# Optimization experiments

Measured on AMD Instinct MI355X. Metric: run time of the kernel, lower is better.

The kernel has to match this reference:

```python
import jax, jax.numpy as jnp
import numpy as np

B, N, DIM = 4, 8192, 512
HEADS, DHEAD = 8, 64
INNER = HEADS * DHEAD          # 512
M = 256                        # num landmarks
L = N // M                     # tokens per landmark group (n % m == 0 -> no pad)
ITERS = 6                      # Moore-Penrose iterations
KRES = 33                      # residual depthwise conv kernel (along n)
SCALE = DHEAD ** -0.5


def setup_inputs() -> dict:
    key = jax.random.key(0)
    k1, k2, k3, k4 = jax.random.split(key, 4)
    return {
        "x": jax.random.normal(k1, (B, N, DIM), jnp.float32),
        "w_qkv": jax.random.normal(k2, (DIM, 3 * INNER), jnp.float32) * (DIM ** -0.5),
        "w_out": jax.random.normal(k3, (INNER, DIM), jnp.float32) * (INNER ** -0.5),
        "b_out": jnp.zeros((DIM,), jnp.float32),
        "res_kernel": jax.random.normal(k4, (HEADS, 1, KRES, 1), jnp.float32) * 0.05,
    }


def _moore_penrose_pinv(x, iters=ITERS):
    # x: (b, h, m, m)
    abs_x = jnp.abs(x)
    col = abs_x.sum(axis=-1)
    row = abs_x.sum(axis=-2)
    z = jnp.swapaxes(x, -1, -2) / (jnp.max(col) * jnp.max(row))
    I = jnp.eye(x.shape[-1], dtype=x.dtype)
    for _ in range(iters):
        xz = x @ z
        z = 0.25 * z @ (13 * I - xz @ (15 * I - xz @ (7 * I - xz)))
    return z


def reference(x, w_qkv, w_out, b_out, res_kernel):
    b, n, _ = x.shape
    qkv = x @ w_qkv                               # (b, n, 3*inner)
    q, k, v = jnp.split(qkv, 3, axis=-1)
    to_heads = lambda t: t.reshape(b, n, HEADS, DHEAD).transpose(0, 2, 1, 3)  # (b,h,n,d)
    q, k, v = to_heads(q), to_heads(k), to_heads(v)
    q = q * SCALE

    # landmarks: mean over consecutive groups of L tokens -> (b,h,M,d)
    q_l = q.reshape(b, HEADS, M, L, DHEAD).sum(axis=3) / L
    k_l = k.reshape(b, HEADS, M, L, DHEAD).sum(axis=3) / L

    attn1 = jax.nn.softmax(jnp.einsum('bhid,bhjd->bhij', q, k_l), axis=-1)    # (b,h,n,M)
    attn2 = jax.nn.softmax(jnp.einsum('bhid,bhjd->bhij', q_l, k_l), axis=-1)  # (b,h,M,M)
    attn3 = jax.nn.softmax(jnp.einsum('bhid,bhjd->bhij', q_l, k), axis=-1)    # (b,h,M,n)

    out = attn1 @ _moore_penrose_pinv(attn2) @ (attn3 @ v)                    # (b,h,n,d)

    # depthwise residual conv over the sequence axis, per head
    res = jax.lax.conv_general_dilated(
        v, res_kernel, window_strides=(1, 1),
        padding=[(KRES // 2, KRES // 2), (0, 0)],
        dimension_numbers=('NCHW', 'OIHW', 'NCHW'),
        feature_group_count=HEADS)
    out = out + res

    out = out.transpose(0, 2, 1, 3).reshape(b, n, INNER)
    return out @ w_out + b_out
```

## Files before the change

### kernel.cpp

```cpp
#include <hip/hip_runtime.h>
#include <stdint.h>
#include <stddef.h>


typedef __bf16 bf16x8 __attribute__((ext_vector_type(8)));
typedef __bf16 bf16x4 __attribute__((ext_vector_type(4)));
typedef float f32x4 __attribute__((ext_vector_type(4)));

__device__ __forceinline__ f32x4 mfma_bf16(bf16x8 a, bf16x8 b, f32x4 c) {
    return __builtin_amdgcn_mfma_f32_16x16x32_bf16(a, b, c, 0, 0, 0);
}

__device__ __forceinline__ void gload16(const __bf16* g, __bf16* l) {
    __builtin_amdgcn_global_load_lds(
        (const __attribute__((address_space(1))) void*)g,
        (__attribute__((address_space(3))) void*)l, 16, 0, 0);
}

__global__ __launch_bounds__(256) void k_cvt(const float* __restrict__ in,
        __bf16* __restrict__ out, float* __restrict__ stats) {
    if (blockIdx.x == 0 && threadIdx.x == 0) { stats[0] = 1.f; stats[1] = 0.f; }
    size_t base = ((size_t)blockIdx.x * 256 + threadIdx.x) * 8;
    float4 a = *(const float4*)&in[base];
    float4 b = *(const float4*)&in[base + 4];
    bf16x8 o;
    o[0] = (__bf16)a.x; o[1] = (__bf16)a.y; o[2] = (__bf16)a.z; o[3] = (__bf16)a.w;
    o[4] = (__bf16)b.x; o[5] = (__bf16)b.y; o[6] = (__bf16)b.z; o[7] = (__bf16)b.w;
    *(bf16x8*)&out[base] = o;
}

__global__ __launch_bounds__(256) void k_transpose_f32(const float* __restrict__ in,
        __bf16* __restrict__ out, int R, int C) {
    __shared__ __bf16 tile[64 * 72];
    int r0 = blockIdx.x * 64, c0 = blockIdx.y * 64;
    int tid = threadIdx.x;
    #pragma unroll
    for (int i = 0; i < 16; ++i) {
        int slot = i * 256 + tid;
        int rr = slot >> 6, cc = slot & 63;
        tile[rr * 72 + cc] = (__bf16)in[(size_t)(r0 + rr) * C + c0 + cc];
    }
    __syncthreads();
    #pragma unroll
    for (int i = 0; i < 2; ++i) {
        int slot = i * 256 + tid;
        int cc = slot >> 3, s = slot & 7;
        bf16x8 t;
        #pragma unroll
        for (int j = 0; j < 8; ++j) t[j] = tile[(s * 8 + j) * 72 + cc];
        *(bf16x8*)&out[(size_t)(c0 + cc) * R + r0 + s * 8] = t;
    }
}

__global__ __launch_bounds__(256) void k_transpose_bf(const __bf16* __restrict__ in,
        __bf16* __restrict__ out, int R, int C, long bsi, long bso) {
    __shared__ __bf16 tile[64 * 72];
    in  += (size_t)blockIdx.z * bsi;
    out += (size_t)blockIdx.z * bso;
    int r0 = blockIdx.x * 64, c0 = blockIdx.y * 64;
    int tid = threadIdx.x;
    #pragma unroll
    for (int i = 0; i < 2; ++i) {
        int slot = i * 256 + tid;
        int rr = slot >> 3, s = slot & 7;
        *(bf16x8*)&tile[rr * 72 + s * 8] =
            *(const bf16x8*)&in[(size_t)(r0 + rr) * C + c0 + s * 8];
    }
    __syncthreads();
    #pragma unroll
    for (int i = 0; i < 2; ++i) {
        int slot = i * 256 + tid;
        int cc = slot >> 3, s = slot & 7;
        bf16x8 t;
        #pragma unroll
        for (int j = 0; j < 8; ++j) t[j] = tile[(s * 8 + j) * 72 + cc];
        *(bf16x8*)&out[(size_t)(c0 + cc) * R + r0 + s * 8] = t;
    }
}

template<int MODE>
__global__ __launch_bounds__(256) void k_gemm_big(const __bf16* __restrict__ A,
        const __bf16* __restrict__ Bt, int K,
        __bf16* __restrict__ qp, __bf16* __restrict__ kp, __bf16* __restrict__ vp,
        float* __restrict__ outp, const float* __restrict__ bias) {
    __shared__ __bf16 sA[128 * 64];
    __shared__ __bf16 sB[128 * 64];
    constexpr int NT  = (MODE == 0) ? 12 : 4;
    constexpr int TOT = (MODE == 0) ? 3072 : 1024;
    int flat = blockIdx.x;
    int t = (flat & 7) * (TOT / 8) + (flat >> 3);
    int m0 = (t / NT) * 128, n0 = (t % NT) * 128;
    int tid = threadIdx.x;
    int wave = tid >> 6, l = tid & 63, lm = l & 15, lq = l >> 4;
    int wm = wave & 1, wn = wave >> 1;
    int lr = l >> 3, lc8 = l & 7;
    int src_c = (lc8 ^ lr) * 8;
    f32x4 acc[4][4] = {};
    for (int k0 = 0; k0 < K; k0 += 64) {
        #pragma unroll
        for (int i = 0; i < 4; ++i) {
            int g = wave * 4 + i;
            gload16(&A[(size_t)(m0 + g * 8 + lr) * K + k0 + src_c], &sA[g * 512]);
        }
        #pragma unroll
        for (int i = 0; i < 4; ++i) {
            int g = wave * 4 + i;
            gload16(&Bt[(size_t)(n0 + g * 8 + lr) * K + k0 + src_c], &sB[g * 512]);
        }
        __syncthreads();
// ... 12 lines not shown
                bfr[ni] = *(bf16x8*)&sB[r * 64 + ((ch ^ (r & 7)) << 3)];
            }
            #pragma unroll
            for (int mi = 0; mi < 4; ++mi)
                #pragma unroll
                for (int ni = 0; ni < 4; ++ni)
                    acc[mi][ni] = mfma_bf16(af[mi], bfr[ni], acc[mi][ni]);
        }
        __syncthreads();
    }
    #pragma unroll
    for (int mi = 0; mi < 4; ++mi)
    #pragma unroll
    for (int ni = 0; ni < 4; ++ni)
    #pragma unroll
    for (int reg = 0; reg < 4; ++reg) {
        int gr = m0 + wm * 64 + mi * 16 + lq * 4 + reg;
        int gc = n0 + wn * 64 + ni * 16 + lm;
        float v = acc[mi][ni][reg];
        if (MODE == 0) {
            int which = gc >> 9, rem = gc & 511;
            int h = rem >> 6, d = rem & 63;
            int b = gr >> 13, tok = gr & 8191;
            size_t dst = ((size_t)((b * 8 + h) * 8192 + tok)) * 64 + d;
            if (which == 0)      qp[dst] = (__bf16)(v * 0.125f);
            else if (which == 1) kp[dst] = (__bf16)v;
            else                 vp[dst] = (__bf16)v;
        } else {
            outp[(size_t)gr * 512 + gc] = v + bias[gc];
        }
    }
}

__global__ __launch_bounds__(256) void k_landmarks(const __bf16* __restrict__ q,
        const __bf16* __restrict__ k, __bf16* __restrict__ ql, __bf16* __restrict__ kl) {
    int idx = blockIdx.x * 256 + threadIdx.x;
    int sel = idx >> 19;
    int rem = idx & 524287;
    int bh = rem >> 14;
    int m  = (rem >> 6) & 255;
    int d  = rem & 63;
    const __bf16* src = sel ? k : q;
    __bf16* dst = sel ? kl : ql;
    const __bf16* p = src + ((size_t)(bh * 8192 + m * 32)) * 64 + d;
    float s = 0.f;
    #pragma unroll
    for (int j = 0; j < 32; ++j) s += (float)p[j * 64];
    dst[(size_t)bh * 16384 + m * 64 + d] = (__bf16)(s * (1.f / 32.f));
}

__global__ __launch_bounds__(256) void k_attn2(const __bf16* __restrict__ ql,
        const __bf16* __restrict__ kl, __bf16* __restrict__ ph, __bf16* __restrict__ pl) {
    int tid = threadIdx.x;
    int wave = tid >> 6, l = tid & 63, lm = l & 15, lq = l >> 4;
    int bh = blockIdx.y;
    int r0 = blockIdx.x * 64 + wave * 16;
    const __bf16* qb = ql + (size_t)bh * 16384;
    const __bf16* kb = kl + (size_t)bh * 16384;
    bf16x8 af[2];
    #pragma unroll
    for (int ko = 0; ko < 2; ++ko)
        af[ko] = *(const bf16x8*)&qb[(size_t)(r0 + lm) * 64 + ko * 32 + lq * 8];
    f32x4 S[16] = {};
    #pragma unroll
    for (int ci = 0; ci < 16; ++ci)
        #pragma unroll
        for (int ko = 0; ko < 2; ++ko) {
            bf16x8 bfr = *(const bf16x8*)&kb[(size_t)(ci * 16 + lm) * 64 + ko * 32 + lq * 8];
            S[ci] = mfma_bf16(af[ko], bfr, S[ci]);
        }
    __bf16* oh = ph + (size_t)bh * 65536;
    __bf16* ol = pl + (size_t)bh * 65536;
    #pragma unroll
    for (int reg = 0; reg < 4; ++reg) {
        float sum = 0.f;
        #pragma unroll
        for (int ci = 0; ci < 16; ++ci) {
            float e = __expf(S[ci][reg]); S[ci][reg] = e; sum += e;
        }
        #pragma unroll
        for (int msk = 1; msk < 16; msk <<= 1) sum += __shfl_xor(sum, msk);
        float inv = 1.f / sum;
        int row = r0 + lq * 4 + reg;
        #pragma unroll
        for (int ci = 0; ci < 16; ++ci) {
            float v = S[ci][reg] * inv;
            __bf16 hh = (__bf16)v;
            oh[(size_t)row * 256 + ci * 16 + lm] = hh;
            ol[(size_t)row * 256 + ci * 16 + lm] = (__bf16)(v - (float)hh);
        }
    }
}

__global__ __launch_bounds__(256) void k_stats(const __bf16* __restrict__ ph,
        const __bf16* __restrict__ pl, float* stats) {
    __shared__ float red[256];
    int tid = threadIdx.x;
    const __bf16* a = ph + (size_t)blockIdx.x * 65536;
    const __bf16* b = pl + (size_t)blockIdx.x * 65536;
    float cs = 0.f;
    for (int r = 0; r < 256; ++r)
        cs += (float)a[r * 256 + tid] + (float)b[r * 256 + tid];
    red[tid] = cs; __syncthreads();
    for (int off = 128; off > 0; off >>= 1) {
        if (tid < off) red[tid] = fmaxf(red[tid], red[tid + off]);
        __syncthreads();
    }
    if (tid == 0) atomicMax((int*)&stats[1], __float_as_int(red[0]));
}

__global__ __launch_bounds__(256) void k_z0(const __bf16* __restrict__ ph,
        const __bf16* __restrict__ pl, const float* __restrict__ stats,
        __bf16* __restrict__ zh, __bf16* __restrict__ zl) {
    int idx = blockIdx.x * 256 + threadIdx.x;
    int bh = idx >> 16, r = (idx >> 8) & 255, c = idx & 255;
    float inv = 1.f / (stats[0] * stats[1]);
    size_t src = ((size_t)bh << 16) + (size_t)c * 256 + r;
    float v = ((float)ph[src] + (float)pl[src]) * inv;
    __bf16 hh = (__bf16)v;
    zh[idx] = hh;
    zl[idx] = (__bf16)(v - (float)hh);
}

__device__ __forceinline__ void pgemm_core(const __bf16* __restrict__ Ah,
        const __bf16* __restrict__ Al, const __bf16* __restrict__ Bth,
        const __bf16* __restrict__ Btl, int m0, int n0,
        __bf16* sAh, __bf16* sAl, __bf16* sBh, __bf16* sBl, f32x4 acc[2]) {
    int tid = threadIdx.x;
    int wave = tid >> 6, l = tid & 63, lm = l & 15, lq = l >> 4;
    int wm = wave & 1, wn = wave >> 1;
    int lr = l >> 3, lc8 = l & 7;
    int src_c = (lc8 ^ lr) * 8;
    for (int k0 = 0; k0 < 256; k0 += 64) {
        {
            size_t ra = (size_t)(m0 + wave * 8 + lr) * 256 + k0 + src_c;
            gload16(&Ah[ra], &sAh[wave * 512]);
            gload16(&Al[ra], &sAl[wave * 512]);
        }
        #pragma unroll
        for (int i = 0; i < 2; ++i) {
            int g = wave * 2 + i;
            size_t rb = (size_t)(n0 + g * 8 + lr) * 256 + k0 + src_c;
            gload16(&Bth[rb], &sBh[g * 512]);
            gload16(&Btl[rb], &sBl[g * 512]);
        }
        __syncthreads();
        #pragma unroll
        for (int ko = 0; ko < 2; ++ko) {
            int ch = (ko << 2) | lq;
            int rA = wm * 16 + lm;
            int oA = rA * 64 + ((ch ^ (rA & 7)) << 3);
            bf16x8 a_h = *(bf16x8*)&sAh[oA];
            bf16x8 a_l = *(bf16x8*)&sAl[oA];
            bf16x8 b_h[2], b_l[2];
            #pragma unroll
            for (int ni = 0; ni < 2; ++ni) {
                int r = wn * 32 + ni * 16 + lm;
                int o = r * 64 + ((ch ^ (r & 7)) << 3);
                b_h[ni] = *(bf16x8*)&sBh[o];
                b_l[ni] = *(bf16x8*)&sBl[o];
            }
            #pragma unroll
            for (int ni = 0; ni < 2; ++ni) {
                acc[ni] = mfma_bf16(a_h, b_h[ni], acc[ni]);
                acc[ni] = mfma_bf16(a_h, b_l[ni], acc[ni]);
                acc[ni] = mfma_bf16(a_l, b_h[ni], acc[ni]);
            }
        }
        __syncthreads();
    }
}

__global__ __launch_bounds__(256) void k_pgemm(const __bf16* __restrict__ Ah,
        const __bf16* __restrict__ Al, const __bf16* __restrict__ Bth,
        const __bf16* __restrict__ Btl, const __bf16* __restrict__ Ch,
        const __bf16* __restrict__ Cl, __bf16* __restrict__ OutH,
        __bf16* __restrict__ OutL, float alpha, const float* __restrict__ sPtr,
        float beta, float delta, int outMode, long bStride) {
    __shared__ __bf16 sAh[32 * 64], sAl[32 * 64], sBh[64 * 64], sBl[64 * 64];
    int tid = threadIdx.x;
    int wave = tid >> 6, l = tid & 63, lm = l & 15, lq = l >> 4;
    int wm = wave & 1, wn = wave >> 1;
    int total = gridDim.x;
    int flat = blockIdx.x;
    int t = (flat & 7) * (total >> 3) + (flat >> 3);
    int ntb = total >> 8;
    int tpb = ntb << 3;
    int bh = t / tpb, rem = t - bh * tpb;
    int m0 = (rem / ntb) * 32, n0 = (rem % ntb) * 64;
    float aEff = alpha;
    if (sPtr) aEff *= 1.f / (sPtr[0] * sPtr[1]);
    f32x4 acc[2] = {};
    pgemm_core(Ah + (size_t)bh * 65536, Al + (size_t)bh * 65536,
               Bth + (size_t)bh * bStride, Btl + (size_t)bh * bStride,
               m0, n0, sAh, sAl, sBh, sBl, acc);
    #pragma unroll
    for (int ni = 0; ni < 2; ++ni)
    #pragma unroll
    for (int reg = 0; reg < 4; ++reg) {
        int gr = m0 + wm * 16 + lq * 4 + reg;
        int gc = n0 + wn * 32 + ni * 16 + lm;
        float v = aEff * acc[ni][reg];
        if (beta != 0.f) {
            size_t ci = (size_t)bh * 65536 + (size_t)gr * 256 + gc;
            v += beta * ((float)Ch[ci] + (float)Cl[ci]);
        }
        if (gr == gc) v += delta;
        if (outMode == 0) {
            size_t di = (size_t)bh * 65536 + (size_t)gr * 256 + gc;
            __bf16 hh = (__bf16)v;
            OutH[di] = hh;
            OutL[di] = (__bf16)(v - (float)hh);
        } else {
            int ci2 = gr >> 4, lqm = (gr >> 2) & 3, r = gr & 3;
            int slot = ((ci2 >> 1) << 5) + (lqm << 3) + ((ci2 & 1) << 2) + r;
            OutH[(size_t)bh * 16384 + (size_t)gc * 256 + slot] = (__bf16)v;
        }
    }
}

__global__ __launch_bounds__(256) void k_pgemm_dual(const __bf16* __restrict__ Zh,
        const __bf16* __restrict__ Zl, const __bf16* __restrict__ A2h,
        const __bf16* __restrict__ A2l, const __bf16* __restrict__ Bth,
        const __bf16* __restrict__ Btl, __bf16* __restrict__ OzH,
        __bf16* __restrict__ OzL, __bf16* __restrict__ OaH, __bf16* __restrict__ OaL) {
    __shared__ __bf16 sAh[32 * 64], sAl[32 * 64], sBh[64 * 64], sBl[64 * 64];
    int tid = threadIdx.x;
    int wave = tid >> 6, l = tid & 63, lm = l & 15, lq = l >> 4;
    int wm = wave & 1, wn = wave >> 1;
    int total = gridDim.x;
    int flat = blockIdx.x;
    int t = (flat & 7) * (total >> 3) + (flat >> 3);
    int zz = t >> 5, rem = t & 31;
    int m0 = (rem >> 2) * 32, n0 = (rem & 3) * 64;
    int bh = zz & 31;
    const __bf16* Lh = (zz >= 32 ? A2h : Zh) + (size_t)bh * 65536;
    const __bf16* Ll = (zz >= 32 ? A2l : Zl) + (size_t)bh * 65536;
    __bf16* Oh = (zz >= 32 ? OaH : OzH) + (size_t)bh * 65536;
    __bf16* Ol = (zz >= 32 ? OaL : OzL) + (size_t)bh * 65536;
    f32x4 acc[2] = {};
    pgemm_core(Lh, Ll, Bth + (size_t)bh * 65536, Btl + (size_t)bh * 65536,
               m0, n0, sAh, sAl, sBh, sBl, acc);
    #pragma unroll
    for (int ni = 0; ni < 2; ++ni)
    #pragma unroll
    for (int reg = 0; reg < 4; ++reg) {
        int gr = m0 + wm * 16 + lq * 4 + reg;
        int gc = n0 + wn * 32 + ni * 16 + lm;
        float v = 0.25f * acc[ni][reg];
        __bf16 hh = (__bf16)v;
        Oh[(size_t)gr * 256 + gc] = hh;
        Ol[(size_t)gr * 256 + gc] = (__bf16)(v - (float)hh);
    }
}

__global__ __launch_bounds__(256) void k_attn3(const __bf16* __restrict__ ql,
        const __bf16* __restrict__ kk, const __bf16* __restrict__ vt,
        float* __restrict__ O_s, float* __restrict__ l_s) {
    int tid = threadIdx.x;
    int wave = tid >> 6, l = tid & 63, lm = l & 15, lq = l >> 4;
    int s = blockIdx.x, bh = blockIdx.y;
    const __bf16* qb = ql + (size_t)bh * 16384;
    bf16x8 qa[4][2];
    #pragma unroll
    for (int mi = 0; mi < 4; ++mi)
        #pragma unroll
        for (int ko = 0; ko < 2; ++ko)
            qa[mi][ko] = *(const bf16x8*)&qb[(size_t)(wave * 64 + mi * 16 + lm) * 64 + ko * 32 + lq * 8];
    f32x4 O[4][4] = {};
    float lsum[4] = {};
    for (int it = 0; it < 8; ++it) {
        int c0 = s * 512 + it * 64;
        bf16x8 kf[4][2];
        #pragma unroll
        for (int ci = 0; ci < 4; ++ci)
            #pragma unroll
            for (int ko = 0; ko < 2; ++ko)
                kf[ci][ko] = *(const bf16x8*)&kk[((size_t)bh * 8192 + c0 + ci * 16 + lm) * 64 + ko * 32 + lq * 8];
        f32x4 St[4][4] = {};
        #pragma unroll
        for (int ci = 0; ci < 4; ++ci)
            #pragma unroll
            for (int ko = 0; ko < 2; ++ko)
                #pragma unroll
                for (int mi = 0; mi < 4; ++mi)
                    St[mi][ci] = mfma_bf16(kf[ci][ko], qa[mi][ko], St[mi][ci]);
        bf16x4 pk[4][4];
        #pragma unroll
        for (int mi = 0; mi < 4; ++mi)
            #pragma unroll
            for (int ci = 0; ci < 4; ++ci)
                #pragma unroll
                for (int reg = 0; reg < 4; ++reg) {
                    float e = __expf(St[mi][ci][reg]);
                    lsum[mi] += e;
                    pk[mi][ci][reg] = (__bf16)e;
                }
        #pragma unroll
        for (int ko = 0; ko < 2; ++ko) {
            bf16x8 af[4];
            #pragma unroll
            for (int mi = 0; mi < 4; ++mi)
                #pragma unroll
                for (int r = 0; r < 4; ++r) {
                    af[mi][r]     = pk[mi][2 * ko][r];
                    af[mi][4 + r] = pk[mi][2 * ko + 1][r];
                }
            #pragma unroll
            for (int ni = 0; ni < 4; ++ni) {
                const __bf16* vrow = &vt[((size_t)bh * 64 + ni * 16 + lm) * 8192 + c0 + ko * 32 + lq * 4];
                bf16x4 v0 = *(const bf16x4*)&vrow[0];
                bf16x4 v1 = *(const bf16x4*)&vrow[16];
                bf16x8 vb;
                #pragma unroll
                for (int r = 0; r < 4; ++r) { vb[r] = v0[r]; vb[4 + r] = v1[r]; }
                #pragma unroll
                for (int mi = 0; mi < 4; ++mi)
                    O[mi][ni] = mfma_bf16(af[mi], vb, O[mi][ni]);
            }
        }
    }
    #pragma unroll
    for (int mi = 0; mi < 4; ++mi) {
        float v = lsum[mi];
        v += __shfl_xor(v, 16);
        v += __shfl_xor(v, 32);
        lsum[mi] = v;
    }
    int base = (bh * 16 + s) * 256;
    #pragma unroll
    for (int mi = 0; mi < 4; ++mi)
        if (lq == 0) l_s[base + wave * 64 + mi * 16 + lm] = lsum[mi];
    #pragma unroll
    for (int mi = 0; mi < 4; ++mi)
        #pragma unroll
        for (int reg = 0; reg < 4; ++reg) {
            int r = wave * 64 + mi * 16 + lq * 4 + reg;
            #pragma unroll
            for (int ni = 0; ni < 4; ++ni)
                O_s[((size_t)(base + r)) * 64 + ni * 16 + lm] = O[mi][ni][reg];
        }
}

__global__ __launch_bounds__(256) void k_t2combine(const float* __restrict__ O_s,
        const float* __restrict__ l_s, __bf16* __restrict__ t2th,
        __bf16* __restrict__ t2tl) {
    int idx = blockIdx.x * 256 + threadIdx.x;
    int bh = idx >> 14, r = (idx >> 6) & 255, d = idx & 63;
    float den = 0.f, num = 0.f;
    #pragma unroll
    for (int s = 0; s < 16; ++s) {
        int b2 = (bh * 16 + s) * 256 + r;
        den += l_s[b2];
        num += O_s[(size_t)b2 * 64 + d];
    }
    float v = num / den;
    __bf16 hh = (__bf16)v;
    size_t di = ((size_t)bh * 64 + d) * 256 + r;
    t2th[di] = hh;
    t2tl[di] = (__bf16)(v - (float)hh);
}

__global__ __launch_bounds__(256) void k_conv(const __bf16* __restrict__ vt,
        const float* __restrict__ resk, __bf16* __restrict__ convb) {
    int bh = blockIdx.y, h = bh & 7;
    int d = threadIdx.x & 63, tg = threadIdx.x >> 6;
    int t0 = blockIdx.x * 64 + tg * 16;
    __shared__ float kfs[33];
    if (threadIdx.x < 33) kfs[threadIdx.x] = resk[h * 33 + threadIdx.x];
    __syncthreads();
    const __bf16* row = vt + ((size_t)bh * 64 + d) * 8192;
    float win[48];
    #pragma unroll
    for (int c = 0; c < 6; ++c) {
        int tok0 = t0 - 16 + c * 8;
        if (tok0 >= 0 && tok0 + 7 < 8192) {
            bf16x8 v8 = *(const bf16x8*)&row[tok0];
            #pragma unroll
            for (int e = 0; e < 8; ++e) win[c * 8 + e] = (float)v8[e];
        } else {
            #pragma unroll
            for (int e = 0; e < 8; ++e) {
                int tok = tok0 + e;
                win[c * 8 + e] = (tok >= 0 && tok < 8192) ? (float)row[tok] : 0.f;
            }
        }
    }
    float o[16];
    #pragma unroll
    for (int i = 0; i < 16; ++i) o[i] = 0.f;
    #pragma unroll
    for (int j = 0; j < 33; ++j) {
        float kf = kfs[j];
        #pragma unroll
        for (int i = 0; i < 16; ++i) o[i] += kf * win[i + j];
    }
    __bf16* outr = convb + ((size_t)bh * 8192) * 64 + d;
    #pragma unroll
    for (int i = 0; i < 16; ++i)
        outr[(size_t)(t0 + i) * 64] = (__bf16)o[i];
}

__global__ __launch_bounds__(256) void k_attn1(const __bf16* __restrict__ q,
        const __bf16* __restrict__ kl, const __bf16* __restrict__ zt2p,
        const __bf16* __restrict__ convb, __bf16* __restrict__ outp) {
    int tid = threadIdx.x;
    int wave = tid >> 6, l = tid & 63, lm = l & 15, lq = l >> 4;
    int bh = blockIdx.y;
    int t0 = blockIdx.x * 256;
    int b = bh >> 3, h = bh & 7;
    const __bf16* qb = q + (size_t)bh * 8192 * 64;
    const __bf16* kb = kl + (size_t)bh * 16384;
    const __bf16* zb = zt2p + (size_t)bh * 16384;
    int rowb = t0 + wave * 64;
    bf16x8 qa[4][2];
    #pragma unroll
    for (int mi = 0; mi < 4; ++mi)
        #pragma unroll
        for (int ko = 0; ko < 2; ++ko)
            qa[mi][ko] = *(const bf16x8*)&qb[(size_t)(rowb + mi * 16 + lm) * 64 + ko * 32 + lq * 8];
    f32x4 O[4][4] = {};
    float rs[4] = {};
    #pragma unroll
    for (int c2 = 0; c2 < 8; ++c2) {
        bf16x8 kf[2][2];
        #pragma unroll
        for (int ci = 0; ci < 2; ++ci)
            #pragma unroll
            for (int ko = 0; ko < 2; ++ko)
                kf[ci][ko] = *(const bf16x8*)&kb[(size_t)((c2 * 2 + ci) * 16 + lm) * 64 + ko * 32 + lq * 8];
        f32x4 St[4][2] = {};
        #pragma unroll
        for (int ci = 0; ci < 2; ++ci)
// ... 67 lines not shown
        off += (bytes + 255) & ~(size_t)255;
        return p;
    };
    const size_t PL = 2097152;
    __bf16* q_bf   = (__bf16*)alloc(33554432);
    __bf16* k_bf   = (__bf16*)alloc(33554432);
    __bf16* vt     = (__bf16*)alloc(33554432);
    __bf16* outpre = (__bf16*)alloc(33554432);
    __bf16* q_l    = (__bf16*)alloc(1048576);
    __bf16* k_l    = (__bf16*)alloc(1048576);
    __bf16* a2h    = (__bf16*)alloc(8388608);
    __bf16* zAh    = (__bf16*)alloc(8388608);
    __bf16* zBh    = (__bf16*)alloc(8388608);
    __bf16* Amh    = (__bf16*)alloc(8388608);
    __bf16* W2h    = (__bf16*)alloc(8388608);
    __bf16* W3h    = (__bf16*)alloc(8388608);
    float*  O_s    = (float*)alloc(33554432);
    float*  l_s    = (float*)alloc(524288);
    __bf16* t2th   = (__bf16*)alloc(2097152);
    __bf16* zt2t   = (__bf16*)alloc(1048576);
    __bf16* wqkvt  = (__bf16*)alloc(1572864);
    __bf16* woutt  = (__bf16*)alloc(524288);
    float*  stats  = (float*)alloc(256);
    __bf16* convb  = (__bf16*)O_s;
    __bf16* xb     = (__bf16*)O_s;
    __bf16* a2l = a2h + PL;
    __bf16* zAl = zAh + PL;
    __bf16* zBl = zBh + PL;
    __bf16* Aml = Amh + PL;
    __bf16* W2l = W2h + PL;
    __bf16* W3l = W3h + PL;
    __bf16* t2tl = t2th + 524288;

    k_cvt<<<8192, 256, 0, stream>>>(x, xb, stats);
    k_transpose_f32<<<dim3(8, 24), 256, 0, stream>>>(wqkv, wqkvt, 512, 1536);
    k_transpose_f32<<<dim3(8, 8), 256, 0, stream>>>(wout, woutt, 512, 512);
    k_gemm_big<0><<<3072, 256, 0, stream>>>(xb, wqkvt, 512,
            q_bf, k_bf, outpre, nullptr, nullptr);
    k_transpose_bf<<<dim3(128, 1, 32), 256, 0, stream>>>(outpre, vt, 8192, 64, 524288, 524288);
    k_landmarks<<<4096, 256, 0, stream>>>(q_bf, k_bf, q_l, k_l);
    k_attn2<<<dim3(4, 32), 256, 0, stream>>>(q_l, k_l, a2h, a2l);
    k_stats<<<32, 256, 0, stream>>>(a2h, a2l, stats);
    k_z0<<<8192, 256, 0, stream>>>(a2h, a2l, stats, zAh, zAl);
    k_attn3<<<dim3(16, 32), 256, 0, stream>>>(q_l, k_bf, vt, O_s, l_s);
    k_t2combine<<<2048, 256, 0, stream>>>(O_s, l_s, t2th, t2tl);
    k_conv<<<dim3(128, 32), 256, 0, stream>>>(vt, resk, convb);
    k_pgemm<<<1024, 256, 0, stream>>>(a2h, a2l, a2h, a2l,
            nullptr, nullptr, Amh, Aml, 1.f, stats, 0.f, 0.f, 0, 65536);
    __bf16 *zch = zAh, *zcl = zAl, *znh = zBh, *znl = zBl;
    __bf16 *Ach = Amh, *Acl = Aml, *Anh = a2h, *Anl = a2l;
    for (int it = 0; it < 6; ++it) {
        k_pgemm<<<1024, 256, 0, stream>>>(Ach, Acl, Ach, Acl,
                Ach, Acl, W2h, W2l, 1.f, nullptr, -7.f, 15.f, 0, 65536);
        k_pgemm<<<1024, 256, 0, stream>>>(Ach, Acl, W2h, W2l,
                nullptr, nullptr, W3h, W3l, -1.f, nullptr, 0.f, 13.f, 0, 65536);
        if (it < 5) {
            k_pgemm_dual<<<2048, 256, 0, stream>>>(zch, zcl, Ach, Acl,
                    W3h, W3l, znh, znl, Anh, Anl);
            __bf16* t;
            t = Ach; Ach = Anh; Anh = t;
            t = Acl; Acl = Anl; Anl = t;
        } else {
            k_pgemm_dual<<<1024, 256, 0, stream>>>(zch, zcl, zch, zcl,
                    W3h, W3l, znh, znl, znh, znl);
        }
        __bf16* t;
        t = zch; zch = znh; znh = t;
        t = zcl; zcl = znl; znl = t;
    }
    k_pgemm<<<256, 256, 0, stream>>>(zch, zcl, t2th, t2tl,
            nullptr, nullptr, zt2t, nullptr, 1.f, nullptr, 0.f, 0.f, 1, 16384);
    k_attn1<<<dim3(32, 32), 256, 0, stream>>>(q_bf, k_l, zt2t, convb, outpre);
    k_gemm_big<1><<<1024, 256, 0, stream>>>(outpre, woutt, 512,
            nullptr, nullptr, nullptr, (float*)d_out, bout);
}
```

Baseline: 642.0 us.

## Merge independent small kernels into combined launches sharing a block-index dispatch

Several independent stages are folded into multi-role kernels that pick their work by block index: input conversion with both weight transposes, the V transpose with landmark pooling, and the attn3/z0/first pgemm, t2combine/W2, and W3/conv pairs. The first iteration's W2 and W3 products are hoisted out of the Newton loop into these combined launches. The aim is to cut launch count and tail idle time by letting unrelated work fill the GPU together. In exchange, heterogeneous blocks share one launch configuration, so register and LDS use is set by the heaviest role and may lower occupancy for the lighter ones.

```diff
diff --git a/kernel.cpp b/kernel.cpp
--- a/kernel.cpp
+++ b/kernel.cpp
@@ -17,10 +17,10 @@
         (__attribute__((address_space(3))) void*)l, 16, 0, 0);
 }
 
-__global__ __launch_bounds__(256) void k_cvt(const float* __restrict__ in,
-        __bf16* __restrict__ out, float* __restrict__ stats) {
-    if (blockIdx.x == 0 && threadIdx.x == 0) { stats[0] = 1.f; stats[1] = 0.f; }
-    size_t base = ((size_t)blockIdx.x * 256 + threadIdx.x) * 8;
+
+__device__ __forceinline__ void cvt_body(int bid, const float* __restrict__ in,
+        __bf16* __restrict__ out) {
+    size_t base = ((size_t)bid * 256 + threadIdx.x) * 8;
     float4 a = *(const float4*)&in[base];
     float4 b = *(const float4*)&in[base + 4];
     bf16x8 o;
@@ -29,10 +29,9 @@
     *(bf16x8*)&out[base] = o;
 }
 
-__global__ __launch_bounds__(256) void k_transpose_f32(const float* __restrict__ in,
-        __bf16* __restrict__ out, int R, int C) {
-    __shared__ __bf16 tile[64 * 72];
-    int r0 = blockIdx.x * 64, c0 = blockIdx.y * 64;
+__device__ __forceinline__ void tf32_body(const float* __restrict__ in,
+        __bf16* __restrict__ out, int R, int C, int bx, int by, __bf16* tile) {
+    int r0 = bx * 64, c0 = by * 64;
     int tid = threadIdx.x;
     #pragma unroll
     for (int i = 0; i < 16; ++i) {
@@ -52,19 +51,18 @@
     }
 }
 
-__global__ __launch_bounds__(256) void k_transpose_bf(const __bf16* __restrict__ in,
-        __bf16* __restrict__ out, int R, int C, long bsi, long bso) {
-    __shared__ __bf16 tile[64 * 72];
-    in  += (size_t)blockIdx.z * bsi;
-    out += (size_t)blockIdx.z * bso;
-    int r0 = blockIdx.x * 64, c0 = blockIdx.y * 64;
+__device__ __forceinline__ void tbf_body(const __bf16* __restrict__ in0,
+        __bf16* __restrict__ out0, int bx, int bz, __bf16* tile) {
+    const __bf16* in = in0 + (size_t)bz * 524288;
+    __bf16* out = out0 + (size_t)bz * 524288;
+    int r0 = bx * 64, c0 = 0;
     int tid = threadIdx.x;
     #pragma unroll
     for (int i = 0; i < 2; ++i) {
         int slot = i * 256 + tid;
         int rr = slot >> 3, s = slot & 7;
         *(bf16x8*)&tile[rr * 72 + s * 8] =
-            *(const bf16x8*)&in[(size_t)(r0 + rr) * C + c0 + s * 8];
+            *(const bf16x8*)&in[(size_t)(r0 + rr) * 64 + c0 + s * 8];
     }
     __syncthreads();
     #pragma unroll
@@ -74,7 +72,293 @@
         bf16x8 t;
         #pragma unroll
         for (int j = 0; j < 8; ++j) t[j] = tile[(s * 8 + j) * 72 + cc];
-        *(bf16x8*)&out[(size_t)(c0 + cc) * R + r0 + s * 8] = t;
+        *(bf16x8*)&out[(size_t)(c0 + cc) * 8192 + r0 + s * 8] = t;
+    }
+}
+
+__device__ __forceinline__ void landmarks_body(int idx, const __bf16* __restrict__ q,
+        const __bf16* __restrict__ k, __bf16* __restrict__ ql, __bf16* __restrict__ kl) {
+    int sel = idx >> 19;
+    int rem = idx & 524287;
+    int bh = rem >> 14;
+    int m  = (rem >> 6) & 255;
+    int d  = rem & 63;
+    const __bf16* src = sel ? k : q;
+    __bf16* dst = sel ? kl : ql;
+    const __bf16* p = src + ((size_t)(bh * 8192 + m * 32)) * 64 + d;
+    float s = 0.f;
+    #pragma unroll
+    for (int j = 0; j < 32; ++j) s += (float)p[j * 64];
+    dst[(size_t)bh * 16384 + m * 64 + d] = (__bf16)(s * (1.f / 32.f));
+}
+
+__device__ __forceinline__ void z0_body(int idx, const __bf16* __restrict__ ph,
+        const __bf16* __restrict__ pl, const float* __restrict__ stats,
+        __bf16* __restrict__ zh, __bf16* __restrict__ zl) {
+    int bh = idx >> 16, r = (idx >> 8) & 255, c = idx & 255;
+    float inv = 1.f / (stats[0] * stats[1]);
+    size_t src = ((size_t)bh << 16) + (size_t)c * 256 + r;
+    float v = ((float)ph[src] + (float)pl[src]) * inv;
+    __bf16 hh = (__bf16)v;
+    zh[idx] = hh;
+    zl[idx] = (__bf16)(v - (float)hh);
+}
+
+__device__ __forceinline__ void pgemm_core(const __bf16* __restrict__ Ah,
+        const __bf16* __restrict__ Al, const __bf16* __restrict__ Bth,
+        const __bf16* __restrict__ Btl, int m0, int n0,
+        __bf16* sAh, __bf16* sAl, __bf16* sBh, __bf16* sBl, f32x4 acc[2]) {
+    int tid = threadIdx.x;
+    int wave = tid >> 6, l = tid & 63, lm = l & 15, lq = l >> 4;
+    int wm = wave & 1, wn = wave >> 1;
+    int lr = l >> 3, lc8 = l & 7;
+    int src_c = (lc8 ^ lr) * 8;
+    for (int k0 = 0; k0 < 256; k0 += 64) {
+        {
+            size_t ra = (size_t)(m0 + wave * 8 + lr) * 256 + k0 + src_c;
+            gload16(&Ah[ra], &sAh[wave * 512]);
+            gload16(&Al[ra], &sAl[wave * 512]);
+        }
+        #pragma unroll
+        for (int i = 0; i < 2; ++i) {
+            int g = wave * 2 + i;
+            size_t rb = (size_t)(n0 + g * 8 + lr) * 256 + k0 + src_c;
+            gload16(&Bth[rb], &sBh[g * 512]);
+            gload16(&Btl[rb], &sBl[g * 512]);
+        }
+        __syncthreads();
+        #pragma unroll
+        for (int ko = 0; ko < 2; ++ko) {
+            int ch = (ko << 2) | lq;
+            int rA = wm * 16 + lm;
+            int oA = rA * 64 + ((ch ^ (rA & 7)) << 3);
+            bf16x8 a_h = *(bf16x8*)&sAh[oA];
+            bf16x8 a_l = *(bf16x8*)&sAl[oA];
+            bf16x8 b_h[2], b_l[2];
+            #pragma unroll
+            for (int ni = 0; ni < 2; ++ni) {
+                int r = wn * 32 + ni * 16 + lm;
+                int o = r * 64 + ((ch ^ (r & 7)) << 3);
+                b_h[ni] = *(bf16x8*)&sBh[o];
+                b_l[ni] = *(bf16x8*)&sBl[o];
+            }
+            #pragma unroll
+            for (int ni = 0; ni < 2; ++ni) {
+                acc[ni] = mfma_bf16(a_h, b_h[ni], acc[ni]);
+                acc[ni] = mfma_bf16(a_h, b_l[ni], acc[ni]);
+                acc[ni] = mfma_bf16(a_l, b_h[ni], acc[ni]);
+            }
+        }
+        __syncthreads();
+    }
+}
+
+__device__ __forceinline__ void pgemm_stage(int flat, int total,
+        const __bf16* __restrict__ Ah, const __bf16* __restrict__ Al,
+        const __bf16* __restrict__ Bth, const __bf16* __restrict__ Btl,
+        const __bf16* __restrict__ Ch, const __bf16* __restrict__ Cl,
+        __bf16* __restrict__ OutH, __bf16* __restrict__ OutL,
+        float aEff, float beta, float delta, int outMode, long bStride,
+        __bf16* sAh, __bf16* sAl, __bf16* sBh, __bf16* sBl) {
+    int tid = threadIdx.x;
+    int wave = tid >> 6, l = tid & 63, lm = l & 15, lq = l >> 4;
+    int wm = wave & 1, wn = wave >> 1;
+    int t = (flat & 7) * (total >> 3) + (flat >> 3);
+    int ntb = total >> 8;
+    int tpb = ntb << 3;
+    int bh = t / tpb, rem = t - bh * tpb;
+    int m0 = (rem / ntb) * 32, n0 = (rem % ntb) * 64;
+    f32x4 acc[2] = {};
+    pgemm_core(Ah + (size_t)bh * 65536, Al + (size_t)bh * 65536,
+               Bth + (size_t)bh * bStride, Btl + (size_t)bh * bStride,
+               m0, n0, sAh, sAl, sBh, sBl, acc);
+    #pragma unroll
+    for (int ni = 0; ni < 2; ++ni)
+    #pragma unroll
+    for (int reg = 0; reg < 4; ++reg) {
+        int gr = m0 + wm * 16 + lq * 4 + reg;
+        int gc = n0 + wn * 32 + ni * 16 + lm;
+        float v = aEff * acc[ni][reg];
+        if (beta != 0.f) {
+            size_t ci = (size_t)bh * 65536 + (size_t)gr * 256 + gc;
+            v += beta * ((float)Ch[ci] + (float)Cl[ci]);
+        }
+        if (gr == gc) v += delta;
+        if (outMode == 0) {
+            size_t di = (size_t)bh * 65536 + (size_t)gr * 256 + gc;
+            __bf16 hh = (__bf16)v;
+            OutH[di] = hh;
+            OutL[di] = (__bf16)(v - (float)hh);
+        } else {
+            int ci2 = gr >> 4, lqm = (gr >> 2) & 3, r = gr & 3;
+            int slot = ((ci2 >> 1) << 5) + (lqm << 3) + ((ci2 & 1) << 2) + r;
+            OutH[(size_t)bh * 16384 + (size_t)gc * 256 + slot] = (__bf16)v;
+        }
+    }
+}
+
+__device__ __forceinline__ void attn3_body(int s, int bh,
+        const __bf16* __restrict__ ql, const __bf16* __restrict__ kk,
+        const __bf16* __restrict__ vt, float* __restrict__ O_s,
+        float* __restrict__ l_s) {
+    int tid = threadIdx.x;
+    int wave = tid >> 6, l = tid & 63, lm = l & 15, lq = l >> 4;
+    const __bf16* qb = ql + (size_t)bh * 16384;
+    bf16x8 qa[4][2];
+    #pragma unroll
+    for (int mi = 0; mi < 4; ++mi)
+        #pragma unroll
+        for (int ko = 0; ko < 2; ++ko)
+            qa[mi][ko] = *(const bf16x8*)&qb[(size_t)(wave * 64 + mi * 16 + lm) * 64 + ko * 32 + lq * 8];
+    f32x4 O[4][4] = {};
+    float lsum[4] = {};
+    for (int it = 0; it < 8; ++it) {
+        int c0 = s * 512 + it * 64;
+        bf16x8 kf[4][2];
+        #pragma unroll
+        for (int ci = 0; ci < 4; ++ci)
+            #pragma unroll
+            for (int ko = 0; ko < 2; ++ko)
+                kf[ci][ko] = *(const bf16x8*)&kk[((size_t)bh * 8192 + c0 + ci * 16 + lm) * 64 + ko * 32 + lq * 8];
+        f32x4 St[4][4] = {};
+        #pragma unroll
+        for (int ci = 0; ci < 4; ++ci)
+            #pragma unroll
+            for (int ko = 0; ko < 2; ++ko)
+                #pragma unroll
+                for (int mi = 0; mi < 4; ++mi)
+                    St[mi][ci] = mfma_bf16(kf[ci][ko], qa[mi][ko], St[mi][ci]);
+        bf16x4 pk[4][4];
+        #pragma unroll
+        for (int mi = 0; mi < 4; ++mi)
+            #pragma unroll
+            for (int ci = 0; ci < 4; ++ci)
+                #pragma unroll
+                for (int reg = 0; reg < 4; ++reg) {
+                    float e = __expf(St[mi][ci][reg]);
+                    lsum[mi] += e;
+                    pk[mi][ci][reg] = (__bf16)e;
+                }
+        #pragma unroll
+        for (int ko = 0; ko < 2; ++ko) {
+            bf16x8 af[4];
+            #pragma unroll
+            for (int mi = 0; mi < 4; ++mi)
+                #pragma unroll
+                for (int r = 0; r < 4; ++r) {
+                    af[mi][r]     = pk[mi][2 * ko][r];
+                    af[mi][4 + r] = pk[mi][2 * ko + 1][r];
+                }
+            #pragma unroll
+            for (int ni = 0; ni < 4; ++ni) {
+                const __bf16* vrow = &vt[((size_t)bh * 64 + ni * 16 + lm) * 8192 + c0 + ko * 32 + lq * 4];
+                bf16x4 v0 = *(const bf16x4*)&vrow[0];
+                bf16x4 v1 = *(const bf16x4*)&vrow[16];
+                bf16x8 vb;
+                #pragma unroll
+                for (int r = 0; r < 4; ++r) { vb[r] = v0[r]; vb[4 + r] = v1[r]; }
+                #pragma unroll
+                for (int mi = 0; mi < 4; ++mi)
+                    O[mi][ni] = mfma_bf16(af[mi], vb, O[mi][ni]);
+            }
+        }
+    }
+    #pragma unroll
+    for (int mi = 0; mi < 4; ++mi) {
+        float v = lsum[mi];
+        v += __shfl_xor(v, 16);
+        v += __shfl_xor(v, 32);
+        lsum[mi] = v;
+    }
+    int base = (bh * 16 + s) * 256;
+    #pragma unroll
+    for (int mi = 0; mi < 4; ++mi)
+        if (lq == 0) l_s[base + wave * 64 + mi * 16 + lm] = lsum[mi];
+    #pragma unroll
+    for (int mi = 0; mi < 4; ++mi)
+        #pragma unroll
+        for (int reg = 0; reg < 4; ++reg) {
+            int r = wave * 64 + mi * 16 + lq * 4 + reg;
+            #pragma unroll
+            for (int ni = 0; ni < 4; ++ni)
+                O_s[((size_t)(base + r)) * 64 + ni * 16 + lm] = O[mi][ni][reg];
+        }
+}
+
+__device__ __forceinline__ void t2c_body(int idx, const float* __restrict__ O_s,
+        const float* __restrict__ l_s, __bf16* __restrict__ t2th,
+        __bf16* __restrict__ t2tl) {
+    int bh = idx >> 14, r = (idx >> 6) & 255, d = idx & 63;
+    float den = 0.f, num = 0.f;
+    #pragma unroll
+    for (int s = 0; s < 16; ++s) {
+        int b2 = (bh * 16 + s) * 256 + r;
+        den += l_s[b2];
+        num += O_s[(size_t)b2 * 64 + d];
+    }
+    float v = num / den;
+    __bf16 hh = (__bf16)v;
+    size_t di = ((size_t)bh * 64 + d) * 256 + r;
+    t2th[di] = hh;
+    t2tl[di] = (__bf16)(v - (float)hh);
+}
+
+__device__ __forceinline__ void conv_body(int bxx, int bh,
+        const __bf16* __restrict__ vt, const float* __restrict__ resk,
+        __bf16* __restrict__ convb, float* kfs) {
+    int h = bh & 7;
+    int d = threadIdx.x & 63, tg = threadIdx.x >> 6;
+    int t0 = bxx * 64 + tg * 16;
+    if (threadIdx.x < 33) kfs[threadIdx.x] = resk[h * 33 + threadIdx.x];
+    __syncthreads();
+    const __bf16* row = vt + ((size_t)bh * 64 + d) * 8192;
+    float win[48];
+    #pragma unroll
+    for (int c = 0; c < 6; ++c) {
+        int tok0 = t0 - 16 + c * 8;
+        if (tok0 >= 0 && tok0 + 7 < 8192) {
+            bf16x8 v8 = *(const bf16x8*)&row[tok0];
+            #pragma unroll
+            for (int e = 0; e < 8; ++e) win[c * 8 + e] = (float)v8[e];
+        } else {
+            #pragma unroll
+            for (int e = 0; e < 8; ++e) {
+                int tok = tok0 + e;
+                win[c * 8 + e] = (tok >= 0 && tok < 8192) ? (float)row[tok] : 0.f;
+            }
+        }
+    }
+    float o[16];
+    #pragma unroll
+    for (int i = 0; i < 16; ++i) o[i] = 0.f;
+    #pragma unroll
+    for (int j = 0; j < 33; ++j) {
+        float kf = kfs[j];
+        #pragma unroll
+        for (int i = 0; i < 16; ++i) o[i] += kf * win[i + j];
+    }
+    __bf16* outr = convb + ((size_t)bh * 8192) * 64 + d;
+    #pragma unroll
+    for (int i = 0; i < 16; ++i)
+        outr[(size_t)(t0 + i) * 64] = (__bf16)o[i];
+}
+
+
+__global__ __launch_bounds__(256) void k_fuse_pre(const float* __restrict__ x,
+        __bf16* __restrict__ xb, float* __restrict__ stats,
+        const float* __restrict__ wqkv, __bf16* __restrict__ wqkvt,
+        const float* __restrict__ wout, __bf16* __restrict__ woutt) {
+    __shared__ __bf16 tile[64 * 72];
+    int id = blockIdx.x;
+    if (id < 8192) {
+        if (id == 0 && threadIdx.x == 0) { stats[0] = 1.f; stats[1] = 0.f; }
+        cvt_body(id, x, xb);
+    } else if (id < 8384) {
+        int lid = id - 8192;
+        tf32_body(wqkv, wqkvt, 512, 1536, lid & 7, lid >> 3, tile);
+    } else {
+        int lid = id - 8384;
+        tf32_body(wout, woutt, 512, 512, lid & 7, lid >> 3, tile);
     }
 }
 
@@ -153,21 +437,17 @@
     }
 }
 
-__global__ __launch_bounds__(256) void k_landmarks(const __bf16* __restrict__ q,
-        const __bf16* __restrict__ k, __bf16* __restrict__ ql, __bf16* __restrict__ kl) {
-    int idx = blockIdx.x * 256 + threadIdx.x;
-    int sel = idx >> 19;
-    int rem = idx & 524287;
-    int bh = rem >> 14;
-    int m  = (rem >> 6) & 255;
-    int d  = rem & 63;
-    const __bf16* src = sel ? k : q;
-    __bf16* dst = sel ? kl : ql;
-    const __bf16* p = src + ((size_t)(bh * 8192 + m * 32)) * 64 + d;
-    float s = 0.f;
-    #pragma unroll
-    for (int j = 0; j < 32; ++j) s += (float)p[j * 64];
-    dst[(size_t)bh * 16384 + m * 64 + d] = (__bf16)(s * (1.f / 32.f));
+__global__ __launch_bounds__(256) void k_fuse_tl(const __bf16* __restrict__ vsrc,
+        __bf16* __restrict__ vt, const __bf16* __restrict__ q,
+        const __bf16* __restrict__ k, __bf16* __restrict__ ql,
+        __bf16* __restrict__ kl) {
+    __shared__ __bf16 tile[64 * 72];
+    int id = blockIdx.x;
+    if (id < 4096) {
+        tbf_body(vsrc, vt, id & 127, id >> 7, tile);
+    } else {
+        landmarks_body((id - 4096) * 256 + threadIdx.x, q, k, ql, kl);
+    }
 }
 
 __global__ __launch_bounds__(256) void k_attn2(const __bf16* __restrict__ ql,
@@ -230,65 +510,56 @@
     if (tid == 0) atomicMax((int*)&stats[1], __float_as_int(red[0]));
 }
 
-__global__ __launch_bounds__(256) void k_z0(const __bf16* __restrict__ ph,
-        const __bf16* __restrict__ pl, const float* __restrict__ stats,
-        __bf16* __restrict__ zh, __bf16* __restrict__ zl) {
-    int idx = blockIdx.x * 256 + threadIdx.x;
-    int bh = idx >> 16, r = (idx >> 8) & 255, c = idx & 255;
-    float inv = 1.f / (stats[0] * stats[1]);
-    size_t src = ((size_t)bh << 16) + (size_t)c * 256 + r;
-    float v = ((float)ph[src] + (float)pl[src]) * inv;
-    __bf16 hh = (__bf16)v;
-    zh[idx] = hh;
-    zl[idx] = (__bf16)(v - (float)hh);
-}
-
-__device__ __forceinline__ void pgemm_core(const __bf16* __restrict__ Ah,
-        const __bf16* __restrict__ Al, const __bf16* __restrict__ Bth,
-        const __bf16* __restrict__ Btl, int m0, int n0,
-        __bf16* sAh, __bf16* sAl, __bf16* sBh, __bf16* sBl, f32x4 acc[2]) {
-    int tid = threadIdx.x;
-    int wave = tid >> 6, l = tid & 63, lm = l & 15, lq = l >> 4;
-    int wm = wave & 1, wn = wave >> 1;
-    int lr = l >> 3, lc8 = l & 7;
-    int src_c = (lc8 ^ lr) * 8;
-    for (int k0 = 0; k0 < 256; k0 += 64) {
-        {
-            size_t ra = (size_t)(m0 + wave * 8 + lr) * 256 + k0 + src_c;
-            gload16(&Ah[ra], &sAh[wave * 512]);
-            gload16(&Al[ra], &sAl[wave * 512]);
-        }
-        #pragma unroll
-        for (int i = 0; i < 2; ++i) {
-            int g = wave * 2 + i;
-            size_t rb = (size_t)(n0 + g * 8 + lr) * 256 + k0 + src_c;
-            gload16(&Bth[rb], &sBh[g * 512]);
-            gload16(&Btl[rb], &sBl[g * 512]);
-        }
-        __syncthreads();
-        #pragma unroll
-        for (int ko = 0; ko < 2; ++ko) {
-            int ch = (ko << 2) | lq;
-            int rA = wm * 16 + lm;
-            int oA = rA * 64 + ((ch ^ (rA & 7)) << 3);
-            bf16x8 a_h = *(bf16x8*)&sAh[oA];
-            bf16x8 a_l = *(bf16x8*)&sAl[oA];
-            bf16x8 b_h[2], b_l[2];
-            #pragma unroll
-            for (int ni = 0; ni < 2; ++ni) {
-                int r = wn * 32 + ni * 16 + lm;
-                int o = r * 64 + ((ch ^ (r & 7)) << 3);
-                b_h[ni] = *(bf16x8*)&sBh[o];
-                b_l[ni] = *(bf16x8*)&sBl[o];
-            }
-            #pragma unroll
-            for (int ni = 0; ni < 2; ++ni) {
-                acc[ni] = mfma_bf16(a_h, b_h[ni], acc[ni]);
-                acc[ni] = mfma_bf16(a_h, b_l[ni], acc[ni]);
-                acc[ni] = mfma_bf16(a_l, b_h[ni], acc[ni]);
-            }
-        }
-        __syncthreads();
+__global__ __launch_bounds__(256) void k_fuse_mid(
+        const __bf16* __restrict__ ql, const __bf16* __restrict__ kbf,
+        const __bf16* __restrict__ vt, float* __restrict__ O_s,
+        float* __restrict__ l_s, const __bf16* __restrict__ a2h,
+        const __bf16* __restrict__ a2l, const float* __restrict__ stats,
+        __bf16* __restrict__ zAh, __bf16* __restrict__ zAl,
+        __bf16* __restrict__ Amh, __bf16* __restrict__ Aml) {
+    __shared__ __bf16 sAh[32 * 64], sAl[32 * 64], sBh[64 * 64], sBl[64 * 64];
+    int id = blockIdx.x;
+    if (id < 512) {
+        attn3_body(id & 15, id >> 4, ql, kbf, vt, O_s, l_s);
+    } else if (id < 8704) {
+        z0_body((id - 512) * 256 + threadIdx.x, a2h, a2l, stats, zAh, zAl);
+    } else {
+        float sc = 1.f / (stats[0] * stats[1]);
+        pgemm_stage(id - 8704, 1024, a2h, a2l, a2h, a2l, nullptr, nullptr,
+                    Amh, Aml, sc, 0.f, 0.f, 0, 65536, sAh, sAl, sBh, sBl);
+    }
+}
+
+__global__ __launch_bounds__(256) void k_fuse_w2t2(
+        const __bf16* __restrict__ Amh, const __bf16* __restrict__ Aml,
+        __bf16* __restrict__ W2h, __bf16* __restrict__ W2l,
+        const float* __restrict__ O_s, const float* __restrict__ l_s,
+        __bf16* __restrict__ t2th, __bf16* __restrict__ t2tl) {
+    __shared__ __bf16 sAh[32 * 64], sAl[32 * 64], sBh[64 * 64], sBl[64 * 64];
+    int id = blockIdx.x;
+    if (id < 1024) {
+        pgemm_stage(id, 1024, Amh, Aml, Amh, Aml, Amh, Aml, W2h, W2l,
+                    1.f, -7.f, 15.f, 0, 65536, sAh, sAl, sBh, sBl);
+    } else {
+        t2c_body((id - 1024) * 256 + threadIdx.x, O_s, l_s, t2th, t2tl);
+    }
+}
+
+__global__ __launch_bounds__(256) void k_fuse_w3conv(
+        const __bf16* __restrict__ Amh, const __bf16* __restrict__ Aml,
+        const __bf16* __restrict__ W2h, const __bf16* __restrict__ W2l,
+        __bf16* __restrict__ W3h, __bf16* __restrict__ W3l,
+        const __bf16* __restrict__ vt, const float* __restrict__ resk,
+        __bf16* __restrict__ convb) {
+    __shared__ __bf16 sAh[32 * 64], sAl[32 * 64], sBh[64 * 64], sBl[64 * 64];
+    __shared__ float kfs[33];
+    int id = blockIdx.x;
+    if (id < 1024) {
+        pgemm_stage(id, 1024, Amh, Aml, W2h, W2l, nullptr, nullptr, W3h, W3l,
+                    -1.f, 0.f, 13.f, 0, 65536, sAh, sAl, sBh, sBl);
+    } else {
+        int lid = id - 1024;
+        conv_body(lid & 127, lid >> 7, vt, resk, convb, kfs);
     }
 }
 
@@ -299,45 +570,10 @@
         __bf16* __restrict__ OutL, float alpha, const float* __restrict__ sPtr,
         float beta, float delta, int outMode, long bStride) {
     __shared__ __bf16 sAh[32 * 64], sAl[32 * 64], sBh[64 * 64], sBl[64 * 64];
-    int tid = threadIdx.x;
-    int wave = tid >> 6, l = tid & 63, lm = l & 15, lq = l >> 4;
-    int wm = wave & 1, wn = wave >> 1;
-    int total = gridDim.x;
-    int flat = blockIdx.x;
-    int t = (flat & 7) * (total >> 3) + (flat >> 3);
-    int ntb = total >> 8;
-    int tpb = ntb << 3;
-    int bh = t / tpb, rem = t - bh * tpb;
-    int m0 = (rem / ntb) * 32, n0 = (rem % ntb) * 64;
     float aEff = alpha;
     if (sPtr) aEff *= 1.f / (sPtr[0] * sPtr[1]);
-    f32x4 acc[2] = {};
-    pgemm_core(Ah + (size_t)bh * 65536, Al + (size_t)bh * 65536,
-               Bth + (size_t)bh * bStride, Btl + (size_t)bh * bStride,
-               m0, n0, sAh, sAl, sBh, sBl, acc);
-    #pragma unroll
-    for (int ni = 0; ni < 2; ++ni)
-    #pragma unroll
-    for (int reg = 0; reg < 4; ++reg) {
-        int gr = m0 + wm * 16 + lq * 4 + reg;
-        int gc = n0 + wn * 32 + ni * 16 + lm;
-        float v = aEff * acc[ni][reg];
-        if (beta != 0.f) {
-            size_t ci = (size_t)bh * 65536 + (size_t)gr * 256 + gc;
-            v += beta * ((float)Ch[ci] + (float)Cl[ci]);
-        }
-        if (gr == gc) v += delta;
-        if (outMode == 0) {
-            size_t di = (size_t)bh * 65536 + (size_t)gr * 256 + gc;
-            __bf16 hh = (__bf16)v;
-            OutH[di] = hh;
-            OutL[di] = (__bf16)(v - (float)hh);
-        } else {
-            int ci2 = gr >> 4, lqm = (gr >> 2) & 3, r = gr & 3;
-            int slot = ((ci2 >> 1) << 5) + (lqm << 3) + ((ci2 & 1) << 2) + r;
-            OutH[(size_t)bh * 16384 + (size_t)gc * 256 + slot] = (__bf16)v;
-        }
-    }
+    pgemm_stage(blockIdx.x, gridDim.x, Ah, Al, Bth, Btl, Ch, Cl, OutH, OutL,
+                aEff, beta, delta, outMode, bStride, sAh, sAl, sBh, sBl);
 }
 
 __global__ __launch_bounds__(256) void k_pgemm_dual(const __bf16* __restrict__ Zh,
@@ -373,153 +609,6 @@
         Oh[(size_t)gr * 256 + gc] = hh;
         Ol[(size_t)gr * 256 + gc] = (__bf16)(v - (float)hh);
     }
-}
-
-__global__ __launch_bounds__(256) void k_attn3(const __bf16* __restrict__ ql,
-        const __bf16* __restrict__ kk, const __bf16* __restrict__ vt,
-        float* __restrict__ O_s, float* __restrict__ l_s) {
-    int tid = threadIdx.x;
-    int wave = tid >> 6, l = tid & 63, lm = l & 15, lq = l >> 4;
-    int s = blockIdx.x, bh = blockIdx.y;
-    const __bf16* qb = ql + (size_t)bh * 16384;
-    bf16x8 qa[4][2];
-    #pragma unroll
-    for (int mi = 0; mi < 4; ++mi)
-        #pragma unroll
-        for (int ko = 0; ko < 2; ++ko)
-            qa[mi][ko] = *(const bf16x8*)&qb[(size_t)(wave * 64 + mi * 16 + lm) * 64 + ko * 32 + lq * 8];
-    f32x4 O[4][4] = {};
-    float lsum[4] = {};
-    for (int it = 0; it < 8; ++it) {
-        int c0 = s * 512 + it * 64;
-        bf16x8 kf[4][2];
-        #pragma unroll
-        for (int ci = 0; ci < 4; ++ci)
-            #pragma unroll
-            for (int ko = 0; ko < 2; ++ko)
-                kf[ci][ko] = *(const bf16x8*)&kk[((size_t)bh * 8192 + c0 + ci * 16 + lm) * 64 + ko * 32 + lq * 8];
-        f32x4 St[4][4] = {};
-        #pragma unroll
-        for (int ci = 0; ci < 4; ++ci)
-            #pragma unroll
-            for (int ko = 0; ko < 2; ++ko)
-                #pragma unroll
-                for (int mi = 0; mi < 4; ++mi)
-                    St[mi][ci] = mfma_bf16(kf[ci][ko], qa[mi][ko], St[mi][ci]);
-        bf16x4 pk[4][4];
-        #pragma unroll
-        for (int mi = 0; mi < 4; ++mi)
-            #pragma unroll
-            for (int ci = 0; ci < 4; ++ci)
-                #pragma unroll
-                for (int reg = 0; reg < 4; ++reg) {
-                    float e = __expf(St[mi][ci][reg]);
-                    lsum[mi] += e;
-                    pk[mi][ci][reg] = (__bf16)e;
-                }
-        #pragma unroll
-        for (int ko = 0; ko < 2; ++ko) {
-            bf16x8 af[4];
-            #pragma unroll
-            for (int mi = 0; mi < 4; ++mi)
-                #pragma unroll
-                for (int r = 0; r < 4; ++r) {
-                    af[mi][r]     = pk[mi][2 * ko][r];
-                    af[mi][4 + r] = pk[mi][2 * ko + 1][r];
-                }
-            #pragma unroll
-            for (int ni = 0; ni < 4; ++ni) {
-                const __bf16* vrow = &vt[((size_t)bh * 64 + ni * 16 + lm) * 8192 + c0 + ko * 32 + lq * 4];
-                bf16x4 v0 = *(const bf16x4*)&vrow[0];
-                bf16x4 v1 = *(const bf16x4*)&vrow[16];
-                bf16x8 vb;
-                #pragma unroll
-                for (int r = 0; r < 4; ++r) { vb[r] = v0[r]; vb[4 + r] = v1[r]; }
-                #pragma unroll
-                for (int mi = 0; mi < 4; ++mi)
-                    O[mi][ni] = mfma_bf16(af[mi], vb, O[mi][ni]);
-            }
-        }
-    }
-    #pragma unroll
-    for (int mi = 0; mi < 4; ++mi) {
-        float v = lsum[mi];
-        v += __shfl_xor(v, 16);
-        v += __shfl_xor(v, 32);
-        lsum[mi] = v;
-    }
-    int base = (bh * 16 + s) * 256;
-    #pragma unroll
-    for (int mi = 0; mi < 4; ++mi)
-        if (lq == 0) l_s[base + wave * 64 + mi * 16 + lm] = lsum[mi];
-    #pragma unroll
-    for (int mi = 0; mi < 4; ++mi)
-        #pragma unroll
-        for (int reg = 0; reg < 4; ++reg) {
-            int r = wave * 64 + mi * 16 + lq * 4 + reg;
-            #pragma unroll
-            for (int ni = 0; ni < 4; ++ni)
-                O_s[((size_t)(base + r)) * 64 + ni * 16 + lm] = O[mi][ni][reg];
-        }
-}
-
-__global__ __launch_bounds__(256) void k_t2combine(const float* __restrict__ O_s,
-        const float* __restrict__ l_s, __bf16* __restrict__ t2th,
-        __bf16* __restrict__ t2tl) {
-    int idx = blockIdx.x * 256 + threadIdx.x;
-    int bh = idx >> 14, r = (idx >> 6) & 255, d = idx & 63;
-    float den = 0.f, num = 0.f;
-    #pragma unroll
-    for (int s = 0; s < 16; ++s) {
-        int b2 = (bh * 16 + s) * 256 + r;
-        den += l_s[b2];
-        num += O_s[(size_t)b2 * 64 + d];
-    }
-    float v = num / den;
-    __bf16 hh = (__bf16)v;
-    size_t di = ((size_t)bh * 64 + d) * 256 + r;
-    t2th[di] = hh;
-    t2tl[di] = (__bf16)(v - (float)hh);
-}
-
-__global__ __launch_bounds__(256) void k_conv(const __bf16* __restrict__ vt,
-        const float* __restrict__ resk, __bf16* __restrict__ convb) {
-    int bh = blockIdx.y, h = bh & 7;
-    int d = threadIdx.x & 63, tg = threadIdx.x >> 6;
-    int t0 = blockIdx.x * 64 + tg * 16;
-    __shared__ float kfs[33];
-    if (threadIdx.x < 33) kfs[threadIdx.x] = resk[h * 33 + threadIdx.x];
-    __syncthreads();
-    const __bf16* row = vt + ((size_t)bh * 64 + d) * 8192;
-    float win[48];
-    #pragma unroll
-    for (int c = 0; c < 6; ++c) {
-        int tok0 = t0 - 16 + c * 8;
-        if (tok0 >= 0 && tok0 + 7 < 8192) {
-            bf16x8 v8 = *(const bf16x8*)&row[tok0];
-            #pragma unroll
-            for (int e = 0; e < 8; ++e) win[c * 8 + e] = (float)v8[e];
-        } else {
-            #pragma unroll
-            for (int e = 0; e < 8; ++e) {
-                int tok = tok0 + e;
-                win[c * 8 + e] = (tok >= 0 && tok < 8192) ? (float)row[tok] : 0.f;
-            }
-        }
-    }
-    float o[16];
-    #pragma unroll
-    for (int i = 0; i < 16; ++i) o[i] = 0.f;
-    #pragma unroll
-    for (int j = 0; j < 33; ++j) {
-        float kf = kfs[j];
-        #pragma unroll
-        for (int i = 0; i < 16; ++i) o[i] += kf * win[i + j];
-    }
-    __bf16* outr = convb + ((size_t)bh * 8192) * 64 + d;
-    #pragma unroll
-    for (int i = 0; i < 16; ++i)
-        outr[(size_t)(t0 + i) * 64] = (__bf16)o[i];
 }
 
 __global__ __launch_bounds__(256) void k_attn1(const __bf16* __restrict__ q,
@@ -653,28 +742,27 @@
     __bf16* W3l = W3h + PL;
     __bf16* t2tl = t2th + 524288;
 
-    k_cvt<<<8192, 256, 0, stream>>>(x, xb, stats);
-    k_transpose_f32<<<dim3(8, 24), 256, 0, stream>>>(wqkv, wqkvt, 512, 1536);
-    k_transpose_f32<<<dim3(8, 8), 256, 0, stream>>>(wout, woutt, 512, 512);
+    k_fuse_pre<<<8448, 256, 0, stream>>>(x, xb, stats, wqkv, wqkvt, wout, woutt);
     k_gemm_big<0><<<3072, 256, 0, stream>>>(xb, wqkvt, 512,
             q_bf, k_bf, outpre, nullptr, nullptr);
-    k_transpose_bf<<<dim3(128, 1, 32), 256, 0, stream>>>(outpre, vt, 8192, 64, 524288, 524288);
-    k_landmarks<<<4096, 256, 0, stream>>>(q_bf, k_bf, q_l, k_l);
+    k_fuse_tl<<<8192, 256, 0, stream>>>(outpre, vt, q_bf, k_bf, q_l, k_l);
     k_attn2<<<dim3(4, 32), 256, 0, stream>>>(q_l, k_l, a2h, a2l);
     k_stats<<<32, 256, 0, stream>>>(a2h, a2l, stats);
-    k_z0<<<8192, 256, 0, stream>>>(a2h, a2l, stats, zAh, zAl);
-    k_attn3<<<dim3(16, 32), 256, 0, stream>>>(q_l, k_bf, vt, O_s, l_s);
-    k_t2combine<<<2048, 256, 0, stream>>>(O_s, l_s, t2th, t2tl);
-    k_conv<<<dim3(128, 32), 256, 0, stream>>>(vt, resk, convb);
-    k_pgemm<<<1024, 256, 0, stream>>>(a2h, a2l, a2h, a2l,
-            nullptr, nullptr, Amh, Aml, 1.f, stats, 0.f, 0.f, 0, 65536);
+    k_fuse_mid<<<9728, 256, 0, stream>>>(q_l, k_bf, vt, O_s, l_s,
+            a2h, a2l, stats, zAh, zAl, Amh, Aml);
+    k_fuse_w2t2<<<3072, 256, 0, stream>>>(Amh, Aml, W2h, W2l, O_s, l_s, t2th, t2tl);
+    k_fuse_w3conv<<<5120, 256, 0, stream>>>(Amh, Aml, W2h, W2l, W3h, W3l,
+            vt, resk, convb);
+
     __bf16 *zch = zAh, *zcl = zAl, *znh = zBh, *znl = zBl;
     __bf16 *Ach = Amh, *Acl = Aml, *Anh = a2h, *Anl = a2l;
     for (int it = 0; it < 6; ++it) {
-        k_pgemm<<<1024, 256, 0, stream>>>(Ach, Acl, Ach, Acl,
-                Ach, Acl, W2h, W2l, 1.f, nullptr, -7.f, 15.f, 0, 65536);
-        k_pgemm<<<1024, 256, 0, stream>>>(Ach, Acl, W2h, W2l,
-                nullptr, nullptr, W3h, W3l, -1.f, nullptr, 0.f, 13.f, 0, 65536);
+        if (it > 0) {
+            k_pgemm<<<1024, 256, 0, stream>>>(Ach, Acl, Ach, Acl,
+                    Ach, Acl, W2h, W2l, 1.f, nullptr, -7.f, 15.f, 0, 65536);
+            k_pgemm<<<1024, 256, 0, stream>>>(Ach, Acl, W2h, W2l,
+                    nullptr, nullptr, W3h, W3l, -1.f, nullptr, 0.f, 13.f, 0, 65536);
+        }
         if (it < 5) {
             k_pgemm_dual<<<2048, 256, 0, stream>>>(zch, zcl, Ach, Acl,
                     W3h, W3l, znh, znl, Anh, Anl);
```

Measured after the change: 618.9 us. -3.6%, faster.
